# Optimization experiments

Hardware: AMD Instinct MI355X
Metric: run time of the kernel (lower is better)

## Reference

```python
import jax, jax.numpy as jnp
import numpy as np

B, CIN, COUT, K, NS, NIN, H = 4, 128, 128, 9, 16384, 16384, 64
W0 = 30.0  # SIREN first-layer frequency


def setup_inputs() -> dict:
    ks = jax.random.split(jax.random.key(0), 8)
    x = jax.random.normal(ks[0], (B, CIN, NIN), dtype=jnp.float32)
    neighbours = jax.random.randint(ks[1], (K, NS), 0, NIN)
    # normalized relative neighbour coordinates in [-1, 1], shape (K*NS, 2)
    coords = 2.0 * jax.random.uniform(ks[2], (K * NS, 2), dtype=jnp.float32) - 1.0
    W1 = jax.random.normal(ks[3], (2, H), dtype=jnp.float32) / jnp.sqrt(2.0)
    b1 = jnp.zeros((H,), dtype=jnp.float32)
    W2 = jax.random.normal(ks[4], (H, H), dtype=jnp.float32) / jnp.sqrt(H * 1.0)
    b2 = jnp.zeros((H,), dtype=jnp.float32)
    W3 = jax.random.normal(ks[5], (H, COUT * CIN), dtype=jnp.float32) / jnp.sqrt(H * 1.0)
    b3 = jnp.zeros((COUT * CIN,), dtype=jnp.float32)
    bias = jnp.zeros((1, COUT, 1), dtype=jnp.float32)
    return {"x": x, "neighbours": neighbours, "coords": coords,
            "W1": W1, "b1": b1, "W2": W2, "b2": b2, "W3": W3, "b3": b3,
            "bias": bias}


def reference(x, neighbours, coords, W1, b1, W2, b2, W3, b3, bias):
    k, ns = neighbours.shape
    cin = x.shape[1]
    cout = W3.shape[1] // cin
    # INR filter generation: (K*NS, 2) -> (K*NS, COUT*CIN)
    h = jnp.sin(W0 * (coords @ W1 + b1))
    h = jnp.sin(h @ W2 + b2)
    f = h @ W3 + b3                                  # (K*NS, COUT*CIN)
    # (K*NS, COUT, CIN) -> (COUT, CIN, K, NS), matching torch permute(1,2,0).reshape
    f = f.reshape(k * ns, cout, cin).transpose(1, 2, 0).reshape(cout, cin, k, ns)
    # neighbor gather: (B, CIN, K, NS)
    x_unfold = x[:, :, neighbours]
    # weighted reduce over (CIN, K) per output location
    out = jnp.einsum('bjkl,ijkl->bil', x_unfold, f)
    return out + bias
```

## Files before the change

### kernel.cpp

```cpp
#include <hip/hip_runtime.h>

#define NS   16384
#define NIN  16384
#define CIN  128
#define COUT 128
#define KNB  9
#define MCH  66
#define QDIM (CIN*MCH)
#define W0C  30.0f

typedef __bf16 bf16;
typedef bf16  bf16x8  __attribute__((ext_vector_type(8)));
typedef bf16  bf16x2  __attribute__((ext_vector_type(2)));
typedef unsigned short u16;
typedef u16   u16x8   __attribute__((ext_vector_type(8)));
typedef float floatx4 __attribute__((ext_vector_type(4)));
typedef unsigned int u32;

__device__ inline u16 f2bf(float f){
  u32 u = __float_as_uint(f);
  u += 0x7fffu + ((u >> 16) & 1u);
  return (u16)(u >> 16);
}
__device__ inline float bf2f(u16 s){
  return __uint_as_float((u32)s << 16);
}
__device__ inline u32 cvtpk2(float lo, float hi){
  u32 r; asm("v_cvt_pk_bf16_f32 %0, %1, %2" : "=v"(r) : "v"(lo), "v"(hi)); return r;
}

#if defined(__has_builtin)
# if __has_builtin(__builtin_amdgcn_fdot2_f32_bf16)
#  define HAVE_DOT2 1
# endif
#endif
#ifndef HAVE_DOT2
# define HAVE_DOT2 0
#endif

__device__ inline float dot2bf(u32 x2, u32 h2, float c){
#if HAVE_DOT2
  return __builtin_amdgcn_fdot2_f32_bf16(__builtin_bit_cast(bf16x2, x2),
                                         __builtin_bit_cast(bf16x2, h2), c, false);
#else
  float xl = bf2f((u16)(x2 & 0xffffu)), xh = bf2f((u16)(x2 >> 16));
  float hl = bf2f((u16)(h2 & 0xffffu)), hh = bf2f((u16)(h2 >> 16));
  return fmaf(xh, hh, fmaf(xl, hl, c));
#endif
}

#define WG_BARRIER() do { \
  asm volatile("s_waitcnt lgkmcnt(0)" ::: "memory"); \
  __builtin_amdgcn_s_barrier(); \
} while (0)

__global__ void k0_vt(const float* __restrict__ W3, const float* __restrict__ b3,
                      u16* __restrict__ Vt){
  int idx = blockIdx.x*256 + threadIdx.x;
  if (idx >= COUT*QDIM) return;
  int i = idx / QDIM;
  int q = idx - i*QDIM;
  int m = q >> 7;
  int j = q & 127;
  float v = 0.f;
  if (m < 64)       v = W3[m*16384 + i*128 + j];
  else if (m == 64) v = b3[i*128 + j];
  Vt[idx] = f2bf(v);
}

__global__ __launch_bounds__(256) void k1h(const float* __restrict__ coords,
      const float* __restrict__ W1, const float* __restrict__ b1,
      const float* __restrict__ W2, const float* __restrict__ b2,
      u32* __restrict__ hK){
  __shared__ u16 sh[KNB][32][66];
  const int tid  = threadIdx.x;
  const int lane = tid & 63;
  const int w    = tid >> 6;
  const int l0   = blockIdx.x*32;
  for (int e = w; e < KNB*32; e += 4){
    int k = e >> 5, l = e & 31;
    int pt = (k << 14) + l0 + l;
    float c0 = coords[2*pt], c1 = coords[2*pt+1];
    float z  = fmaf(c0, W1[lane], fmaf(c1, W1[64+lane], b1[lane]));
    float h1 = sinf(W0C * z);
    float acc = b2[lane];
    #pragma unroll
    for (int mp = 0; mp < 64; ++mp)
      acc = fmaf(__shfl(h1, mp, 64), W2[mp*64 + lane], acc);
    sh[k][l][lane] = f2bf(sinf(acc));
    if (lane == 0){ sh[k][l][64] = 0x3F80; sh[k][l][65] = 0; }
  }
  __syncthreads();
  for (int e = tid; e < 66*5*32; e += 256){
    int m  = e / 160;
    int r  = e - m*160;
    int kp = r >> 5;
    int l  = r & 31;
    u32 lo = sh[2*kp][l][m];
    u32 hi = (kp < 4) ? (u32)sh[2*kp+1][l][m] : 0u;
    hK[(((size_t)m*5 + kp) << 14) + l0 + l] = lo | (hi << 16);
  }
}

__global__ void k_tr(const float* __restrict__ x, u16* __restrict__ xT){
  __shared__ __align__(16) float t[32][33];
  int b  = blockIdx.z;
  int j0 = blockIdx.y*32;
  int p0 = blockIdx.x*32;
  int tx = threadIdx.x, ty = threadIdx.y;
  const float* xb  = x  + (size_t)b*CIN*NIN;
  u16*         xTb = xT + (size_t)b*NIN*CIN;
  #pragma unroll
  for (int n = 0; n < 4; ++n)
    t[ty+8*n][tx] = xb[(size_t)(j0+ty+8*n)*NIN + p0+tx];
  __syncthreads();
  #pragma unroll
  for (int n = 0; n < 4; ++n)
    xTb[(size_t)(p0+ty+8*n)*CIN + j0+tx] = f2bf(t[tx][ty+8*n]);
}

__global__ __launch_bounds__(512, 4) void k_fused(
      const u16* __restrict__ xT,
      const u32* __restrict__ hK,
      const int* __restrict__ nb,
      const u16* __restrict__ Vt,
      const float* __restrict__ bias,
      float* __restrict__ out){
  __shared__ __align__(16) u16 A[2][2][32][136];
  __shared__ u32 hs[2][2][5][32];
  __shared__ int pk[KNB][32];

  const int tid = threadIdx.x;
  const int r0  = blockIdx.x * 32;
  const int b   = r0 >> 14;
  const int l0  = r0 & (NS-1);

  if (tid < KNB*32){
    int k = tid >> 5, l = tid & 31;
    pk[k][l] = nb[k*NS + l0 + l];
  }
  WG_BARRIER();

  const int lq = tid >> 4;
  const int jc = tid & 15;

  const bool hact = tid < 320;
  const int  hs_  = tid / 160;
  const int  hr_  = tid - hs_*160;
  const int  hkp_ = hr_ >> 5;
  const int  hl_  = hr_ & 31;
  const u32* hKp  = hK + (((size_t)(5*hs_ + hkp_)) << 14) + l0 + hl_;
  const size_t HSTR = (size_t)10 << 14;
  u32 hra = 0, hrb = 0;
  if (hact){
    u32 h0 = hKp[0];
    hra = hKp[HSTR];
    hrb = hKp[2*HSTR];
    hs[0][hs_][hkp_][hl_] = h0;
  }

  const char* xbB = (const char*)(xT + ((size_t)b << 21));
  u32 xp[5][8];
  #pragma unroll
  for (int kp = 0; kp < 4; ++kp){
    u16x8 ga = *(const u16x8*)(xbB + (((size_t)(u32)pk[2*kp  ][lq]) << 8) + (size_t)jc*16);
    u16x8 gb = *(const u16x8*)(xbB + (((size_t)(u32)pk[2*kp+1][lq]) << 8) + (size_t)jc*16);
    #pragma unroll
    for (int j = 0; j < 8; ++j) xp[kp][j] = (u32)ga[j] | ((u32)gb[j] << 16);
  }
  {
    u16x8 ga = *(const u16x8*)(xbB + (((size_t)(u32)pk[8][lq]) << 8) + (size_t)jc*16);
    #pragma unroll
    for (int j = 0; j < 8; ++j) xp[4][j] = (u32)ga[j];
  }

  const int lane  = tid & 63;
  const int w     = tid >> 6;
  const int iq    = w & 3;
  const int kh    = w >> 2;
  const int ar    = lane & 15;
  const int klane = lane >> 4;

  floatx4 acc[2][2];
  #pragma unroll
  for (int r = 0; r < 2; ++r)
    #pragma unroll
    for (int f = 0; f < 2; ++f)
      acc[r][f] = (floatx4){0.f,0.f,0.f,0.f};

  const char* VtB0 = (const char*)Vt + (size_t)(iq*32      + ar)*(QDIM*2) + (size_t)(kh*128 + klane*16);
  const char* VtB1 = (const char*)Vt + (size_t)(iq*32 + 16 + ar)*(QDIM*2) + (size_t)(kh*128 + klane*16);

  bf16x8 bv[2][4];
  #pragma unroll
  for (int mm = 0; mm < 2; ++mm)
    #pragma unroll
    for (int kt = 0; kt < 2; ++kt){
      bv[0][mm*2+kt] = *(const bf16x8*)(VtB0 + mm*256 + kt*64);
      bv[1][mm*2+kt] = *(const bf16x8*)(VtB1 + mm*256 + kt*64);
    }

  WG_BARRIER();

  for (int mg = 0; mg < 33; ++mg){
    const int pb = mg & 1;

    float a2[2][8];
    #pragma unroll
    for (int s = 0; s < 2; ++s)
      #pragma unroll
      for (int j = 0; j < 8; ++j) a2[s][j] = 0.f;
    #pragma unroll
    for (int s = 0; s < 2; ++s){
      #pragma unroll
      for (int kp = 0; kp < 5; ++kp){
        u32 hp = hs[pb][s][kp][lq];
        #pragma unroll
        for (int j = 0; j < 8; ++j)
          a2[s][j] = dot2bf(xp[kp][j], hp, a2[s][j]);
      }
    }
    {
      uint4 q0, q1;
      q0.x = cvtpk2(a2[0][0], a2[0][1]); q0.y = cvtpk2(a2[0][2], a2[0][3]);
      q0.z = cvtpk2(a2[0][4], a2[0][5]); q0.w = cvtpk2(a2[0][6], a2[0][7]);
      q1.x = cvtpk2(a2[1][0], a2[1][1]); q1.y = cvtpk2(a2[1][2], a2[1][3]);
      q1.z = cvtpk2(a2[1][4], a2[1][5]); q1.w = cvtpk2(a2[1][6], a2[1][7]);
      *(uint4*)&A[pb][0][lq][jc*8] = q0;
      *(uint4*)&A[pb][1][lq][jc*8] = q1;
    }

    if (hact){
      if (mg < 32) hs[pb^1][hs_][hkp_][hl_] = hra;
      hra = hrb;
      if (mg <= 29) hrb = hKp[(size_t)(mg+3)*HSTR];
    }

    WG_BARRIER();

    __builtin_amdgcn_s_setprio(1);
    #pragma unroll
    for (int mm = 0; mm < 2; ++mm){
      const char* Ab = (const char*)&A[pb][mm][0][0] + kh*128 + klane*16;
      #pragma unroll
      for (int kt = 0; kt < 2; ++kt){
        bf16x8 av0 = *(const bf16x8*)(Ab + (     ar)*272 + kt*64);
        bf16x8 av1 = *(const bf16x8*)(Ab + (16 + ar)*272 + kt*64);
        acc[0][0] = __builtin_amdgcn_mfma_f32_16x16x32_bf16(av0, bv[0][mm*2+kt], acc[0][0], 0, 0, 0);
        acc[0][1] = __builtin_amdgcn_mfma_f32_16x16x32_bf16(av0, bv[1][mm*2+kt], acc[0][1], 0, 0, 0);
        acc[1][0] = __builtin_amdgcn_mfma_f32_16x16x32_bf16(av1, bv[0][mm*2+kt], acc[1][0], 0, 0, 0);
        acc[1][1] = __builtin_amdgcn_mfma_f32_16x16x32_bf16(av1, bv[1][mm*2+kt], acc[1][1], 0, 0, 0);
      }
    }
    __builtin_amdgcn_s_setprio(0);

    if (mg < 32){
      const char* Vg0 = VtB0 + (size_t)(mg+1)*512;
      const char* Vg1 = VtB1 + (size_t)(mg+1)*512;
      #pragma unroll
      for (int mm = 0; mm < 2; ++mm)
        #pragma unroll
        for (int kt = 0; kt < 2; ++kt){
          bv[0][mm*2+kt] = *(const bf16x8*)(Vg0 + mm*256 + kt*64);
          bv[1][mm*2+kt] = *(const bf16x8*)(Vg1 + mm*256 + kt*64);
        }
    }
  }

  WG_BARRIER();
  floatx4* red = (floatx4*)&A[0][0][0][0];
  if (kh == 1){
    floatx4* dst = red + (((size_t)iq*64 + lane) << 2);
    dst[0] = acc[0][0]; dst[1] = acc[0][1]; dst[2] = acc[1][0]; dst[3] = acc[1][1];
  }
  WG_BARRIER();
  if (kh == 0){
    const floatx4* src = red + (((size_t)iq*64 + lane) << 2);
    acc[0][0] += src[0]; acc[0][1] += src[1];
    acc[1][0] += src[2]; acc[1][1] += src[3];
    float* ob = out + ((size_t)b << 21);
    #pragma unroll
    for (int rf = 0; rf < 2; ++rf){
      #pragma unroll
      for (int f = 0; f < 2; ++f){
        int i = iq*32 + f*16 + ar;
        float bi = bias[i];
        int l = l0 + rf*16 + klane*4;
        float4 v;
        v.x = acc[rf][f][0] + bi;
        v.y = acc[rf][f][1] + bi;
        v.z = acc[rf][f][2] + bi;
        v.w = acc[rf][f][3] + bi;
        *(float4*)(ob + ((size_t)i << 14) + l) = v;
      }
    }
  }
}

__global__ __launch_bounds__(256) void k_naive(const float* __restrict__ x,
      const int* __restrict__ nb, const float* __restrict__ coords,
      const float* __restrict__ W1, const float* __restrict__ b1,
      const float* __restrict__ W2, const float* __restrict__ b2,
      const float* __restrict__ W3, const float* __restrict__ b3,
      const float* __restrict__ bias, float* __restrict__ out){
  __shared__ __align__(16) float hk[KNB][68];
  __shared__ int pk[KNB];
  __shared__ __align__(16) float xg[4][KNB][128];
  __shared__ __align__(16) float ul[128][66];
  int tid = threadIdx.x;
  int l = blockIdx.x;
  int lane = tid & 63, wid = tid >> 6;
  if (tid < KNB) pk[tid] = nb[tid*NS + l];
  for (int k = wid; k < KNB; k += 4){
    int pt = k*NS + l;
    float c0 = coords[2*pt], c1 = coords[2*pt+1];
    float z  = fmaf(c0, W1[lane], fmaf(c1, W1[64+lane], b1[lane]));
    float h1 = sinf(W0C*z);
    float a = b2[lane];
    for (int mp = 0; mp < 64; ++mp)
      a = fmaf(__shfl(h1, mp, 64), W2[mp*64+lane], a);
    hk[k][lane] = sinf(a);
    if (lane == 0){ hk[k][64] = 1.f; hk[k][65] = 0.f; }
  }
  __syncthreads();
  for (int idx = tid; idx < 4*KNB*128; idx += 256){
    int b = idx / (KNB*128);
    int r = idx - b*KNB*128;
    int k = r >> 7;
    int j = r & 127;
    xg[b][k][j] = x[((size_t)b*CIN + j)*NIN + pk[k]];
  }
  __syncthreads();
  for (int b = 0; b < 4; ++b){
    for (int idx = tid; idx < 128*65; idx += 256){
      int j = idx / 65, m = idx - j*65;
      float s = 0.f;
      for (int k = 0; k < KNB; ++k) s = fmaf(xg[b][k][j], hk[k][m], s);
      ul[j][m] = s;
    }
    __syncthreads();
    if (tid < 128){
      int i = tid;
      float v = bias[i];
      for (int j = 0; j < 128; ++j){
        const float* wcol = W3 + i*128 + j;
        for (int m = 0; m < 64; ++m)
          v = fmaf(ul[j][m], wcol[(size_t)m*16384], v);
        v = fmaf(ul[j][64], b3[i*128+j], v);
      }
      out[((size_t)b<<21) + ((size_t)i<<14) + l] = v;
    }
    __syncthreads();
  }
}

extern "C" void kernel_launch(void* const* d_in, const int* in_sizes, int n_in,
                              void* d_out, int out_size, void* d_ws, size_t ws_size,
                              hipStream_t stream) {
  const float* x      = (const float*)d_in[0];
  const int*   nb     = (const int*)  d_in[1];
  const float* coords = (const float*)d_in[2];
  const float* W1     = (const float*)d_in[3];
  const float* b1     = (const float*)d_in[4];
  const float* W2     = (const float*)d_in[5];
  const float* b2     = (const float*)d_in[6];
  const float* W3     = (const float*)d_in[7];
  const float* b3     = (const float*)d_in[8];
  const float* bias   = (const float*)d_in[9];
  float* out = (float*)d_out;

  const size_t VT_BYTES = (size_t)COUT*QDIM*2;
  const size_t HK_BYTES = (size_t)MCH*5*NS*4;
  const size_t XT_BYTES = (size_t)4*NIN*CIN*2;
  const size_t FIXED    = VT_BYTES + HK_BYTES + XT_BYTES;

  if (ws_size >= FIXED) {
    char* ws = (char*)d_ws;
    unsigned short* Vt = (unsigned short*)ws;
    u32*            hK = (u32*)(ws + VT_BYTES);
    unsigned short* xT = (unsigned short*)(ws + VT_BYTES + HK_BYTES);

    k0_vt<<<(COUT*QDIM + 255)/256, 256, 0, stream>>>(W3, b3, Vt);
    k1h<<<NS/32, 256, 0, stream>>>(coords, W1, b1, W2, b2, hK);
    k_tr<<<dim3(NIN/32, CIN/32, 4), dim3(32, 8), 0, stream>>>(x, xT);
    k_fused<<<(4*NS)/32, 512, 0, stream>>>(xT, hK, nb, Vt, bias, out);
  } else {
    k_naive<<<NS, 256, 0, stream>>>(x, nb, coords, W1, b1, W2, b2, W3, b3, bias, out);
  }
  (void)in_sizes; (void)n_in; (void)out_size;
}
```

Before: 702.3 us.

## Warp-specialize fused kernel into producer builders and MFMA consumer waves

```diff
diff --git a/kernel.cpp b/kernel.cpp
--- a/kernel.cpp
+++ b/kernel.cpp
@@ -51,7 +51,9 @@
 
 #define WG_BARRIER() do { \
   asm volatile("s_waitcnt lgkmcnt(0)" ::: "memory"); \
+  __builtin_amdgcn_sched_barrier(0); \
   __builtin_amdgcn_s_barrier(); \
+  __builtin_amdgcn_sched_barrier(0); \
 } while (0)
 
 __global__ void k0_vt(const float* __restrict__ W3, const float* __restrict__ b3,
@@ -68,7 +70,7 @@
   Vt[idx] = f2bf(v);
 }
 
-__global__ __launch_bounds__(256) void k1h(const float* __restrict__ coords,
+__global__ __launch_bounds__(1024) void k1h(const float* __restrict__ coords,
       const float* __restrict__ W1, const float* __restrict__ b1,
       const float* __restrict__ W2, const float* __restrict__ b2,
       u32* __restrict__ hK){
@@ -77,7 +79,7 @@
   const int lane = tid & 63;
   const int w    = tid >> 6;
   const int l0   = blockIdx.x*32;
-  for (int e = w; e < KNB*32; e += 4){
+  for (int e = w; e < KNB*32; e += 16){
     int k = e >> 5, l = e & 31;
     int pt = (k << 14) + l0 + l;
     float c0 = coords[2*pt], c1 = coords[2*pt+1];
@@ -91,7 +93,7 @@
     if (lane == 0){ sh[k][l][64] = 0x3F80; sh[k][l][65] = 0; }
   }
   __syncthreads();
-  for (int e = tid; e < 66*5*32; e += 256){
+  for (int e = tid; e < 66*5*32; e += 1024){
     int m  = e / 160;
     int r  = e - m*160;
     int kp = r >> 5;
@@ -127,7 +129,6 @@
       const float* __restrict__ bias,
       float* __restrict__ out){
   __shared__ __align__(16) u16 A[2][2][32][136];
-  __shared__ u32 hs[2][2][5][32];
   __shared__ int pk[KNB][32];
 
   const int tid = threadIdx.x;
@@ -141,143 +142,138 @@
   }
   WG_BARRIER();
 
-  const int lq = tid >> 4;
-  const int jc = tid & 15;
-
-  const bool hact = tid < 320;
-  const int  hs_  = tid / 160;
-  const int  hr_  = tid - hs_*160;
-  const int  hkp_ = hr_ >> 5;
-  const int  hl_  = hr_ & 31;
-  const u32* hKp  = hK + (((size_t)(5*hs_ + hkp_)) << 14) + l0 + hl_;
-  const size_t HSTR = (size_t)10 << 14;
-  u32 hra = 0, hrb = 0;
-  if (hact){
-    u32 h0 = hKp[0];
-    hra = hKp[HSTR];
-    hrb = hKp[2*HSTR];
-    hs[0][hs_][hkp_][hl_] = h0;
-  }
-
-  const char* xbB = (const char*)(xT + ((size_t)b << 21));
-  u32 xp[5][8];
-  #pragma unroll
-  for (int kp = 0; kp < 4; ++kp){
-    u16x8 ga = *(const u16x8*)(xbB + (((size_t)(u32)pk[2*kp  ][lq]) << 8) + (size_t)jc*16);
-    u16x8 gb = *(const u16x8*)(xbB + (((size_t)(u32)pk[2*kp+1][lq]) << 8) + (size_t)jc*16);
-    #pragma unroll
-    for (int j = 0; j < 8; ++j) xp[kp][j] = (u32)ga[j] | ((u32)gb[j] << 16);
-  }
-  {
-    u16x8 ga = *(const u16x8*)(xbB + (((size_t)(u32)pk[8][lq]) << 8) + (size_t)jc*16);
-    #pragma unroll
-    for (int j = 0; j < 8; ++j) xp[4][j] = (u32)ga[j];
-  }
-
-  const int lane  = tid & 63;
-  const int w     = tid >> 6;
-  const int iq    = w & 3;
-  const int kh    = w >> 2;
-  const int ar    = lane & 15;
-  const int klane = lane >> 4;
-
-  floatx4 acc[2][2];
-  #pragma unroll
-  for (int r = 0; r < 2; ++r)
-    #pragma unroll
-    for (int f = 0; f < 2; ++f)
-      acc[r][f] = (floatx4){0.f,0.f,0.f,0.f};
-
-  const char* VtB0 = (const char*)Vt + (size_t)(iq*32      + ar)*(QDIM*2) + (size_t)(kh*128 + klane*16);
-  const char* VtB1 = (const char*)Vt + (size_t)(iq*32 + 16 + ar)*(QDIM*2) + (size_t)(kh*128 + klane*16);
-
-  bf16x8 bv[2][4];
-  #pragma unroll
-  for (int mm = 0; mm < 2; ++mm)
-    #pragma unroll
-    for (int kt = 0; kt < 2; ++kt){
-      bv[0][mm*2+kt] = *(const bf16x8*)(VtB0 + mm*256 + kt*64);
-      bv[1][mm*2+kt] = *(const bf16x8*)(VtB1 + mm*256 + kt*64);
-    }
-
-  WG_BARRIER();
-
-  for (int mg = 0; mg < 33; ++mg){
-    const int pb = mg & 1;
-
-    float a2[2][8];
-    #pragma unroll
-    for (int s = 0; s < 2; ++s)
-      #pragma unroll
-      for (int j = 0; j < 8; ++j) a2[s][j] = 0.f;
-    #pragma unroll
-    for (int s = 0; s < 2; ++s){
-      #pragma unroll
-      for (int kp = 0; kp < 5; ++kp){
-        u32 hp = hs[pb][s][kp][lq];
+  const int w = tid >> 6;
+
+  if (w >= 4){
+    const int ptid = tid - 256;
+    const int lq   = ptid >> 3;
+    const int jc2  = ptid & 7;
+
+    const u32* hKb = hK + l0 + lq;
+    u32 hA[10], hB[10];
+    #pragma unroll
+    for (int t = 0; t < 10; ++t) hA[t] = hKb[(size_t)(t) << 14];
+    #pragma unroll
+    for (int t = 0; t < 10; ++t) hB[t] = hKb[(size_t)(10 + t) << 14];
+
+    const char* xbB = (const char*)(xT + ((size_t)b << 21));
+    u32 xp[5][16];
+    #pragma unroll
+    for (int kp = 0; kp < 4; ++kp){
+      const char* ra = xbB + (((size_t)(u32)pk[2*kp  ][lq]) << 8) + (size_t)jc2*32;
+      const char* rb = xbB + (((size_t)(u32)pk[2*kp+1][lq]) << 8) + (size_t)jc2*32;
+      u16x8 a0 = *(const u16x8*)(ra);
+      u16x8 a1 = *(const u16x8*)(ra + 16);
+      u16x8 b0 = *(const u16x8*)(rb);
+      u16x8 b1 = *(const u16x8*)(rb + 16);
+      #pragma unroll
+      for (int j = 0; j < 8; ++j){
+        xp[kp][j]   = (u32)a0[j] | ((u32)b0[j] << 16);
+        xp[kp][j+8] = (u32)a1[j] | ((u32)b1[j] << 16);
+      }
+    }
+    {
+      const char* ra = xbB + (((size_t)(u32)pk[8][lq]) << 8) + (size_t)jc2*32;
+      u16x8 a0 = *(const u16x8*)(ra);
+      u16x8 a1 = *(const u16x8*)(ra + 16);
+      #pragma unroll
+      for (int j = 0; j < 8; ++j){ xp[4][j] = a0[j]; xp[4][j+8] = a1[j]; }
+    }
+
+    auto build = [&](int buf, const u32 (&H)[10]){
+      #pragma unroll
+      for (int s = 0; s < 2; ++s){
         #pragma unroll
-        for (int j = 0; j < 8; ++j)
-          a2[s][j] = dot2bf(xp[kp][j], hp, a2[s][j]);
-      }
-    }
-    {
-      uint4 q0, q1;
-      q0.x = cvtpk2(a2[0][0], a2[0][1]); q0.y = cvtpk2(a2[0][2], a2[0][3]);
-      q0.z = cvtpk2(a2[0][4], a2[0][5]); q0.w = cvtpk2(a2[0][6], a2[0][7]);
-      q1.x = cvtpk2(a2[1][0], a2[1][1]); q1.y = cvtpk2(a2[1][2], a2[1][3]);
-      q1.z = cvtpk2(a2[1][4], a2[1][5]); q1.w = cvtpk2(a2[1][6], a2[1][7]);
-      *(uint4*)&A[pb][0][lq][jc*8] = q0;
-      *(uint4*)&A[pb][1][lq][jc*8] = q1;
-    }
-
-    if (hact){
-      if (mg < 32) hs[pb^1][hs_][hkp_][hl_] = hra;
-      hra = hrb;
-      if (mg <= 29) hrb = hKp[(size_t)(mg+3)*HSTR];
-    }
-
+        for (int jh = 0; jh < 2; ++jh){
+          float a2[8];
+          #pragma unroll
+          for (int j = 0; j < 8; ++j) a2[j] = 0.f;
+          #pragma unroll
+          for (int kp = 0; kp < 5; ++kp){
+            u32 hp = H[s*5 + kp];
+            #pragma unroll
+            for (int j = 0; j < 8; ++j)
+              a2[j] = dot2bf(xp[kp][jh*8 + j], hp, a2[j]);
+          }
+          uint4 q;
+          q.x = cvtpk2(a2[0], a2[1]); q.y = cvtpk2(a2[2], a2[3]);
+          q.z = cvtpk2(a2[4], a2[5]); q.w = cvtpk2(a2[6], a2[7]);
+          *(uint4*)&A[buf][s][lq][jc2*16 + jh*8] = q;
+        }
+      }
+    };
+
+    build(0, hA);
+    #pragma unroll
+    for (int t = 0; t < 10; ++t) hA[t] = hKb[(size_t)(20 + t) << 14];
     WG_BARRIER();
 
-    __builtin_amdgcn_s_setprio(1);
-    #pragma unroll
-    for (int mm = 0; mm < 2; ++mm){
-      const char* Ab = (const char*)&A[pb][mm][0][0] + kh*128 + klane*16;
-      #pragma unroll
-      for (int kt = 0; kt < 2; ++kt){
-        bf16x8 av0 = *(const bf16x8*)(Ab + (     ar)*272 + kt*64);
-        bf16x8 av1 = *(const bf16x8*)(Ab + (16 + ar)*272 + kt*64);
-        acc[0][0] = __builtin_amdgcn_mfma_f32_16x16x32_bf16(av0, bv[0][mm*2+kt], acc[0][0], 0, 0, 0);
-        acc[0][1] = __builtin_amdgcn_mfma_f32_16x16x32_bf16(av0, bv[1][mm*2+kt], acc[0][1], 0, 0, 0);
-        acc[1][0] = __builtin_amdgcn_mfma_f32_16x16x32_bf16(av1, bv[0][mm*2+kt], acc[1][0], 0, 0, 0);
-        acc[1][1] = __builtin_amdgcn_mfma_f32_16x16x32_bf16(av1, bv[1][mm*2+kt], acc[1][1], 0, 0, 0);
-      }
-    }
-    __builtin_amdgcn_s_setprio(0);
-
-    if (mg < 32){
-      const char* Vg0 = VtB0 + (size_t)(mg+1)*512;
-      const char* Vg1 = VtB1 + (size_t)(mg+1)*512;
-      #pragma unroll
-      for (int mm = 0; mm < 2; ++mm)
+    for (int mg = 0; mg < 33; mg += 2){
+      if (mg < 32) build(1, hB);
+      if (mg + 3 <= 32){
         #pragma unroll
-        for (int kt = 0; kt < 2; ++kt){
-          bv[0][mm*2+kt] = *(const bf16x8*)(Vg0 + mm*256 + kt*64);
-          bv[1][mm*2+kt] = *(const bf16x8*)(Vg1 + mm*256 + kt*64);
+        for (int t = 0; t < 10; ++t) hB[t] = hKb[(size_t)((mg+3)*10 + t) << 14];
+      }
+      WG_BARRIER();
+      if (mg + 1 < 33){
+        if (mg + 1 < 32) build(0, hA);
+        if (mg + 4 <= 32){
+          #pragma unroll
+          for (int t = 0; t < 10; ++t) hA[t] = hKb[(size_t)((mg+4)*10 + t) << 14];
         }
-    }
-  }
-
-  WG_BARRIER();
-  floatx4* red = (floatx4*)&A[0][0][0][0];
-  if (kh == 1){
-    floatx4* dst = red + (((size_t)iq*64 + lane) << 2);
-    dst[0] = acc[0][0]; dst[1] = acc[0][1]; dst[2] = acc[1][0]; dst[3] = acc[1][1];
-  }
-  WG_BARRIER();
-  if (kh == 0){
-    const floatx4* src = red + (((size_t)iq*64 + lane) << 2);
-    acc[0][0] += src[0]; acc[0][1] += src[1];
-    acc[1][0] += src[2]; acc[1][1] += src[3];
+        WG_BARRIER();
+      }
+    }
+  } else {
+    const int lane  = tid & 63;
+    const int iq    = w;
+    const int ar    = lane & 15;
+    const int klane = lane >> 4;
+
+    floatx4 acc[2][2];
+    #pragma unroll
+    for (int r = 0; r < 2; ++r)
+      #pragma unroll
+      for (int f = 0; f < 2; ++f)
+        acc[r][f] = (floatx4){0.f,0.f,0.f,0.f};
+
+    const char* VtB0 = (const char*)Vt + (size_t)(iq*32      + ar)*(QDIM*2) + (size_t)klane*16;
+    const char* VtB1 = (const char*)Vt + (size_t)(iq*32 + 16 + ar)*(QDIM*2) + (size_t)klane*16;
+
+    bf16x8 bvv[2][4][2];
+    #pragma unroll
+    for (int mm = 0; mm < 2; ++mm)
+      #pragma unroll
+      for (int kt = 0; kt < 4; ++kt){
+        bvv[mm][kt][0] = *(const bf16x8*)(VtB0 + mm*256 + kt*64);
+        bvv[mm][kt][1] = *(const bf16x8*)(VtB1 + mm*256 + kt*64);
+      }
+
+    WG_BARRIER();
+
+    for (int mg = 0; mg < 33; ++mg){
+      const int pb = mg & 1;
+      const size_t nxt = (size_t)(mg + 1) * 512;
+      __builtin_amdgcn_s_setprio(1);
+      #pragma unroll
+      for (int mm = 0; mm < 2; ++mm){
+        const char* Ab = (const char*)&A[pb][mm][0][0] + (size_t)klane*16;
+        #pragma unroll
+        for (int kt = 0; kt < 4; ++kt){
+          bf16x8 av0 = *(const bf16x8*)(Ab + (     ar)*272 + kt*64);
+          bf16x8 av1 = *(const bf16x8*)(Ab + (16 + ar)*272 + kt*64);
+          acc[0][0] = __builtin_amdgcn_mfma_f32_16x16x32_bf16(av0, bvv[mm][kt][0], acc[0][0], 0, 0, 0);
+          acc[0][1] = __builtin_amdgcn_mfma_f32_16x16x32_bf16(av0, bvv[mm][kt][1], acc[0][1], 0, 0, 0);
+          acc[1][0] = __builtin_amdgcn_mfma_f32_16x16x32_bf16(av1, bvv[mm][kt][0], acc[1][0], 0, 0, 0);
+          acc[1][1] = __builtin_amdgcn_mfma_f32_16x16x32_bf16(av1, bvv[mm][kt][1], acc[1][1], 0, 0, 0);
+          bvv[mm][kt][0] = *(const bf16x8*)(VtB0 + nxt + mm*256 + kt*64);
+          bvv[mm][kt][1] = *(const bf16x8*)(VtB1 + nxt + mm*256 + kt*64);
+        }
+      }
+      __builtin_amdgcn_s_setprio(0);
+      WG_BARRIER();
+    }
+
     float* ob = out + ((size_t)b << 21);
     #pragma unroll
     for (int rf = 0; rf < 2; ++rf){
@@ -369,7 +365,7 @@
   const float* bias   = (const float*)d_in[9];
   float* out = (float*)d_out;
 
-  const size_t VT_BYTES = (size_t)COUT*QDIM*2;
+  const size_t VT_BYTES = (size_t)COUT*QDIM*2 + 4096;
   const size_t HK_BYTES = (size_t)MCH*5*NS*4;
   const size_t XT_BYTES = (size_t)4*NIN*CIN*2;
   const size_t FIXED    = VT_BYTES + HK_BYTES + XT_BYTES;
@@ -381,7 +377,7 @@
     unsigned short* xT = (unsigned short*)(ws + VT_BYTES + HK_BYTES);
 
     k0_vt<<<(COUT*QDIM + 255)/256, 256, 0, stream>>>(W3, b3, Vt);
-    k1h<<<NS/32, 256, 0, stream>>>(coords, W1, b1, W2, b2, hK);
+    k1h<<<NS/32, 1024, 0, stream>>>(coords, W1, b1, W2, b2, hK);
     k_tr<<<dim3(NIN/32, CIN/32, 4), dim3(32, 8), 0, stream>>>(x, xT);
     k_fused<<<(4*NS)/32, 512, 0, stream>>>(xT, hK, nb, Vt, bias, out);
   } else {
```

Result: slower. 724.4 us (+3.2%).
